# Kernel tuning notes

Hardware: AMD Instinct MI355X
Metric: run time of the kernel (lower is better)

## Reference

```python
import jax, jax.numpy as jnp
import numpy as np

TEMP = 0.3
K_ANCHORS = 512
SK_ITERS = 4  # max_iter=4 in the original; tol early-exit omitted (fixed small iter count)
EPS = 1e-12   # F.normalize clamp_min eps


def setup_inputs() -> dict:
    key = jax.random.key(0)
    k1, k2 = jax.random.split(key)
    x = jax.random.normal(k1, (16, 256, 64, 64), dtype=jnp.float32)
    some_idx = jax.random.randint(k2, (K_ANCHORS,), 0, 64 * 64, dtype=jnp.int32)
    return {"x": x, "some_idx": some_idx}


def sinkhorn_knopp(A):
    # A: [M, k], strictly positive. Normalize by total mass, then alternate
    # L1 column / row normalization (p=1 normalize on positive entries == sum-divide).
    A = A / A.sum()
    def body(A, _):
        A = A / jnp.clip(A.sum(axis=0, keepdims=True), EPS)  # columns
        A = A / jnp.clip(A.sum(axis=1, keepdims=True), EPS)  # rows
        return A, None
    A, _ = jax.lax.scan(body, A, None, length=SK_ITERS)
    return A


def reference(x, some_idx):
    N, C, H, W = x.shape
    k = some_idx.shape[0]
    # L2-normalize over channel dim (F.normalize dim=1)
    l2_x = x / jnp.clip(jnp.linalg.norm(x, axis=1, keepdims=True), EPS)
    # gather k random spatial anchors -> [N, C, k]
    some_x = jnp.take(l2_x.reshape(N, C, H * W), some_idx, axis=-1)
    # cosine scores [N, k, H, W]
    scores = jnp.einsum('nchw,nck->nkhw', l2_x, some_x)
    # flatten to [N*H*W, k], exponentiate, Sinkhorn-Knopp
    A = jnp.exp(scores.transpose(0, 2, 3, 1).reshape(-1, k) / TEMP)
    A = sinkhorn_knopp(A)
    Kmat = A.reshape(N, H, W, k).transpose(0, 3, 1, 2)  # [N, k, H, W]
    # reconstruct from anchors
    return jnp.einsum('nkhw,nck->nchw', Kmat, some_x)
```

## Files before the change

### kernel.cpp

```cpp
#include <hip/hip_runtime.h>
#include <hip/hip_bf16.h>
#include <hip/hip_fp16.h>

#define N_B 16
#define C_DIM 256
#define HW 4096
#define M_TOT (N_B*HW)
#define K_A 512
#define TEMP_INV (1.0f/0.3f)
#define EPS_SK 1e-12f

typedef _Float16 f16x8 __attribute__((ext_vector_type(8)));
typedef _Float16 f16x4 __attribute__((ext_vector_type(4)));
typedef float f32x4 __attribute__((ext_vector_type(4)));

#define GLOBAL_AS __attribute__((address_space(1)))
#define LDS_AS __attribute__((address_space(3)))
__device__ __forceinline__ void gload_lds16(const void* g, void* l){
    __builtin_amdgcn_global_load_lds((GLOBAL_AS const void*)g, (LDS_AS void*)l, 16, 0, 0);
}

__global__ __launch_bounds__(256) void k_normtrans(const float* __restrict__ x,
                                                   _Float16* __restrict__ Lt,
                                                   float* __restrict__ u,
                                                   float* __restrict__ v){
    __shared__ float tl[64][257];
    __shared__ float red[4][64];
    __shared__ float invs[64];
    int n   = blockIdx.x >> 6;
    int hw0 = (blockIdx.x & 63) * 64;
    if (threadIdx.x < 64) u[blockIdx.x*64 + threadIdx.x] = 1.0f;
    if (blockIdx.x < 2)   v[blockIdx.x*256 + threadIdx.x] = 1.0f;
    int tx4 = threadIdx.x & 15;
    int cy  = threadIdx.x >> 4;
    const float* px = x + ((size_t)(n*C_DIM + cy))*HW + hw0 + tx4*4;
    #pragma unroll
    for (int r = 0; r < 16; ++r){
        float4 xv = *(const float4*)(px + (size_t)(r*16)*HW);
        int c = cy + r*16;
        tl[tx4*4+0][c] = xv.x;
        tl[tx4*4+1][c] = xv.y;
        tl[tx4*4+2][c] = xv.z;
        tl[tx4*4+3][c] = xv.w;
    }
    __syncthreads();
    int tx = threadIdx.x & 63, ty = threadIdx.x >> 6;
    float ss = 0.f;
    #pragma unroll
    for (int cc = 0; cc < 64; ++cc){
        float tv = tl[tx][cc*4 + ty];
        ss += tv*tv;
    }
    red[ty][tx] = ss;
    __syncthreads();
    if (ty == 0){
        float s = red[0][tx]+red[1][tx]+red[2][tx]+red[3][tx];
        invs[tx] = 1.0f / fmaxf(sqrtf(s), 1e-12f);
    }
    __syncthreads();
    #pragma unroll
    for (int r = 0; r < 16; ++r){
        int hwl = ty + r*4;
        float inv = invs[hwl];
        float4 a = *(const float4*)&tl[hwl][tx*4];
        f16x4 h;
        h[0] = (_Float16)(a.x*inv); h[1] = (_Float16)(a.y*inv);
        h[2] = (_Float16)(a.z*inv); h[3] = (_Float16)(a.w*inv);
        *(f16x4*)&Lt[((size_t)(n*HW + hw0 + hwl))*C_DIM + tx*4] = h;
    }
}

__global__ __launch_bounds__(256) void k_gather(const _Float16* __restrict__ Lt,
                                                const int* __restrict__ sidx,
                                                _Float16* __restrict__ sxT){
    int n  = blockIdx.y;
    int jj = blockIdx.x*8 + (threadIdx.x >> 5);
    int c8 = (threadIdx.x & 31) * 8;
    int p  = sidx[jj];
    *(f16x8*)&sxT[((size_t)(n*K_A + jj))*C_DIM + c8] =
        *(const f16x8*)&Lt[((size_t)(n*HW + p))*C_DIM + c8];
}

__global__ __launch_bounds__(256) void k_gemm1(const _Float16* __restrict__ Lt,
                                               const _Float16* __restrict__ sxT,
                                               _Float16* __restrict__ A0,
                                               float* __restrict__ part){
    __shared__ _Float16 As[3*128*32];
    __shared__ _Float16 Bs[3*128*32];
    __shared__ float colred[4][128];
    const int swz = (blockIdx.x & 7)*256 + (blockIdx.x >> 3);
    const int jb = swz & 3, mb = (swz >> 2) & 31, nb = swz >> 7;
    const int mbase = mb * 128;
    const int jbase = jb * 128;
    const int t = threadIdx.x;
    const int lane = t & 63, w = t >> 6;
    const int wm = (w >> 1)*64, wn = (w & 1)*64;
    const int l15 = lane & 15, lq = lane >> 4;

    f32x4 acc[4][4] = {};
    const _Float16* pa = Lt  + ((size_t)(nb*HW  + mbase))*C_DIM;
    const _Float16* pb = sxT + ((size_t)(nb*K_A + jbase))*C_DIM;

    const int r0 = t >> 2, ch = t & 3;
    const int r1 = r0 + 64;
    const int cs0 = (ch ^ ((r0 >> 1) & 3)) << 3;
    const int cs1 = (ch ^ ((r1 >> 1) & 3)) << 3;

#define STAGE1(buf, kt) { int k0 = (kt)*32; \
    gload_lds16(pa + (size_t)r0*C_DIM + k0 + cs0, &As[(buf)*4096 + t*8]); \
    gload_lds16(pa + (size_t)r1*C_DIM + k0 + cs1, &As[(buf)*4096 + (256+t)*8]); \
    gload_lds16(pb + (size_t)r0*C_DIM + k0 + cs0, &Bs[(buf)*4096 + t*8]); \
    gload_lds16(pb + (size_t)r1*C_DIM + k0 + cs1, &Bs[(buf)*4096 + (256+t)*8]); }

    STAGE1(0, 0); STAGE1(1, 1); STAGE1(2, 2);
    #pragma unroll
    for (int kt = 0; kt < 8; ++kt){
        if (kt < 6)      asm volatile("s_waitcnt vmcnt(8)" ::: "memory");
        else if (kt < 7) asm volatile("s_waitcnt vmcnt(4)" ::: "memory");
        else             asm volatile("s_waitcnt vmcnt(0)" ::: "memory");
        __builtin_amdgcn_s_barrier();
        __builtin_amdgcn_sched_barrier(0);
        const int cur = kt % 3;
        f16x8 af[4], bf[4];
        #pragma unroll
        for (int mi = 0; mi < 4; ++mi){
            int r = wm + mi*16 + l15;
            af[mi] = *(const f16x8*)&As[cur*4096 + r*32 + ((lq ^ ((r>>1)&3)) << 3)];
        }
        #pragma unroll
        for (int ni = 0; ni < 4; ++ni){
            int r = wn + ni*16 + l15;
            bf[ni] = *(const f16x8*)&Bs[cur*4096 + r*32 + ((lq ^ ((r>>1)&3)) << 3)];
        }
        #pragma unroll
        for (int mi = 0; mi < 4; ++mi)
            #pragma unroll
            for (int ni = 0; ni < 4; ++ni)
                acc[mi][ni] = __builtin_amdgcn_mfma_f32_16x16x32_f16(af[mi], bf[ni], acc[mi][ni], 0, 0, 0);
        __builtin_amdgcn_s_barrier();
        __builtin_amdgcn_sched_barrier(0);
        if (kt < 5) STAGE1((kt+3)%3, kt+3);
    }
    float csum[4] = {0.f, 0.f, 0.f, 0.f};
    #pragma unroll
    for (int mi = 0; mi < 4; ++mi)
        #pragma unroll
        for (int ni = 0; ni < 4; ++ni)
            #pragma unroll
            for (int r = 0; r < 4; ++r){
                int hw = mbase + wm + mi*16 + lq*4 + r;
                int j  = jbase + wn + ni*16 + l15;
                float e = __expf(acc[mi][ni][r] * TEMP_INV);
                A0[((size_t)(nb*HW + hw))*K_A + j] = (_Float16)e;
                csum[ni] += e;
            }
    #pragma unroll
    for (int ni = 0; ni < 4; ++ni){
        float cv = csum[ni];
        cv += __shfl_xor(cv, 16);
        cv += __shfl_xor(cv, 32);
        if (lane < 16) colred[w][wn + ni*16 + l15] = cv;
    }
    __syncthreads();
    if (t < 128){
        int jj = t;
        float s = (jj < 64) ? (colred[0][jj] + colred[2][jj])
                            : (colred[1][jj] + colred[3][jj]);
        part[((size_t)(nb*32 + mb))*K_A + jbase + jj] = s;
    }
}

__global__ __launch_bounds__(64) void k_colfinish(const float* __restrict__ part,
                                                  float* __restrict__ v, int nchunks){
    int j = blockIdx.x;
    int lane = threadIdx.x;
    float s = 0.f;
    for (int r = lane; r < nchunks; r += 64) s += part[(size_t)r*K_A + j];
    #pragma unroll
    for (int off = 32; off; off >>= 1) s += __shfl_xor(s, off);
    if (lane == 0){
        float vo = v[j];
        v[j] = 128.0f * vo / fmaxf(vo * s, EPS_SK);
    }
}

__global__ __launch_bounds__(256) void k_fused(const _Float16* __restrict__ A0,
                                               const float* __restrict__ v,
                                               float* __restrict__ u,
                                               float* __restrict__ part){
    __shared__ float red[4][512];
    int b = blockIdx.x;
    int tg = threadIdx.x >> 6, lane = threadIdx.x & 63;
    float vr[8];
    const float* pv = v + (lane << 3);
    #pragma unroll
    for (int e = 0; e < 8; ++e) vr[e] = pv[e];
    float acc[8] = {};
    for (int it = 0; it < 16; ++it){
        int i = (b << 6) + (it << 2) + tg;
        f16x8 a = *(const f16x8*)&A0[(size_t)i*K_A + (lane << 3)];
        float r = 0.f;
        #pragma unroll
        for (int e = 0; e < 8; ++e) r += (float)a[e] * vr[e];
        #pragma unroll
        for (int off = 32; off; off >>= 1) r += __shfl_xor(r, off);
        float uo = u[i];
        float un = uo / fmaxf(uo * r, EPS_SK);
        if (lane == 0) u[i] = un;
        #pragma unroll
        for (int e = 0; e < 8; ++e) acc[e] += (float)a[e] * un;
    }
    #pragma unroll
    for (int e = 0; e < 8; ++e) red[tg][(lane<<3)+e] = acc[e];
    __syncthreads();
    if (tg == 0){
        #pragma unroll
        for (int e = 0; e < 8; ++e){
            int j = (lane<<3)+e;
            part[((size_t)b)*K_A + j] = red[0][j]+red[1][j]+red[2][j]+red[3][j];
        }
    }
}

__global__ __launch_bounds__(256) void k_sxvT(const _Float16* __restrict__ sxT,
                                              const float* __restrict__ v,
                                              _Float16* __restrict__ SXv){
    __shared__ float tl[64][65];
    int n  = blockIdx.z;
    int j0 = blockIdx.x * 64;
    int c0 = blockIdx.y * 64;
    int tx = threadIdx.x & 63, ty = threadIdx.x >> 6;
    #pragma unroll
    for (int r = 0; r < 16; ++r){
        int jl = ty + r*4;
        tl[jl][tx] = (float)sxT[((size_t)(n*K_A + j0 + jl))*C_DIM + c0 + tx] * v[j0 + jl];
    }
    __syncthreads();
    #pragma unroll
    for (int r = 0; r < 16; ++r){
        int cl = ty + r*4;
        SXv[((size_t)(n*C_DIM + c0 + cl))*K_A + j0 + tx] = (_Float16)tl[tx][cl];
    }
}

__global__ __launch_bounds__(256) void k_gemm2(const _Float16* __restrict__ SXv,
                                               const _Float16* __restrict__ A0,
                                               const float* __restrict__ v,
                                               const float* __restrict__ u,
                                               float* __restrict__ out){
    __shared__ _Float16 As[3*128*32];
    __shared__ _Float16 Bs[3*128*32];
    __shared__ _Float16 vsh[512];
    const int swz = (blockIdx.x & 7)*128 + (blockIdx.x >> 3);
    const int mb = swz & 1, nbi = (swz >> 1) & 31, nb = swz >> 6;
    const int mbase = mb * 128;
    const int nbase = nbi * 128;
    const int t = threadIdx.x;
    const int lane = t & 63, w = t >> 6;
    const int wm = (w >> 1)*64, wn = (w & 1)*64;
    const int l15 = lane & 15, lq = lane >> 4;

    vsh[t]       = (_Float16)v[t];
    vsh[t + 256] = (_Float16)v[t + 256];

    f32x4 acc[4][4] = {};
    f32x4 racc[4] = {};
    const _Float16* pa = SXv + ((size_t)(nb*C_DIM + mbase))*K_A;
    const _Float16* pb = A0  + ((size_t)(nb*HW   + nbase))*K_A;

    const int r0 = t >> 2, ch = t & 3;
    const int r1 = r0 + 64;
    const int cs0 = (ch ^ ((r0 >> 1) & 3)) << 3;
    const int cs1 = (ch ^ ((r1 >> 1) & 3)) << 3;

#define STAGE2(buf, kt) { int k0 = (kt)*32; \
    gload_lds16(pa + (size_t)r0*K_A + k0 + cs0, &As[(buf)*4096 + t*8]); \
    gload_lds16(pa + (size_t)r1*K_A + k0 + cs1, &As[(buf)*4096 + (256+t)*8]); \
    gload_lds16(pb + (size_t)r0*K_A + k0 + cs0, &Bs[(buf)*4096 + t*8]); \
    gload_lds16(pb + (size_t)r1*K_A + k0 + cs1, &Bs[(buf)*4096 + (256+t)*8]); }

    STAGE2(0, 0); STAGE2(1, 1); STAGE2(2, 2);
    #pragma unroll
    for (int kt = 0; kt < 16; ++kt){
        if (kt < 14)      asm volatile("s_waitcnt vmcnt(8)" ::: "memory");
        else if (kt < 15) asm volatile("s_waitcnt vmcnt(4)" ::: "memory");
        else              asm volatile("s_waitcnt vmcnt(0)" ::: "memory");
        __builtin_amdgcn_s_barrier();
        __builtin_amdgcn_sched_barrier(0);
        const int cur = kt % 3;
        f16x8 af[4], bf[4], vf;
        vf = *(const f16x8*)&vsh[kt*32 + lq*8];
        #pragma unroll
        for (int mi = 0; mi < 4; ++mi){
            int r = wm + mi*16 + l15;
            af[mi] = *(const f16x8*)&As[cur*4096 + r*32 + ((lq ^ ((r>>1)&3)) << 3)];
        }
        #pragma unroll
        for (int ni = 0; ni < 4; ++ni){
            int r = wn + ni*16 + l15;
            bf[ni] = *(const f16x8*)&Bs[cur*4096 + r*32 + ((lq ^ ((r>>1)&3)) << 3)];
        }
        #pragma unroll
        for (int mi = 0; mi < 4; ++mi)
            #pragma unroll
            for (int ni = 0; ni < 4; ++ni)
                acc[mi][ni] = __builtin_amdgcn_mfma_f32_16x16x32_f16(af[mi], bf[ni], acc[mi][ni], 0, 0, 0);
        #pragma unroll
        for (int ni = 0; ni < 4; ++ni)
            racc[ni] = __builtin_amdgcn_mfma_f32_16x16x32_f16(vf, bf[ni], racc[ni], 0, 0, 0);
        __builtin_amdgcn_s_barrier();
        __builtin_amdgcn_sched_barrier(0);
        if (kt < 13) STAGE2((kt+3)%3, kt+3);
    }
    float un[4];
    #pragma unroll
    for (int ni = 0; ni < 4; ++ni){
        float rv = racc[ni][0];
        float uo = u[nb*HW + nbase + wn + ni*16 + l15];
        un[ni] = uo / fmaxf(uo * rv, EPS_SK);
    }
    #pragma unroll
    for (int mi = 0; mi < 4; ++mi)
        #pragma unroll
        for (int ni = 0; ni < 4; ++ni)
            #pragma unroll
            for (int r = 0; r < 4; ++r){
                int c  = mbase + wm + mi*16 + lq*4 + r;
                int hw = nbase + wn + ni*16 + l15;
                out[((size_t)(nb*C_DIM + c))*HW + hw] = acc[mi][ni][r] * un[ni];
            }
}

extern "C" void kernel_launch(void* const* d_in, const int* in_sizes, int n_in,
                              void* d_out, int out_size, void* d_ws, size_t ws_size,
                              hipStream_t stream){
    const float* x  = (const float*)d_in[0];
    const int* sidx = (const int*)d_in[1];
    float* out = (float*)d_out;

    char* ws = (char*)d_ws;
    _Float16* Lt  = (_Float16*)ws;  ws += (size_t)N_B*HW*C_DIM*2;
    _Float16* A0  = (_Float16*)ws;  ws += (size_t)M_TOT*K_A*2;
    _Float16* sxT = (_Float16*)ws;  ws += (size_t)N_B*K_A*C_DIM*2;
    _Float16* SXv = (_Float16*)ws;  ws += (size_t)N_B*C_DIM*K_A*2;
    float*    u   = (float*)ws;     ws += (size_t)M_TOT*4;
    float*    v   = (float*)ws;     ws += (size_t)K_A*4;
    float*    part= (float*)ws;     ws += (size_t)1024*K_A*4;

    k_normtrans<<<1024, 256, 0, stream>>>(x, Lt, u, v);
    k_gather   <<<dim3(64,16), 256, 0, stream>>>(Lt, sidx, sxT);
    k_gemm1    <<<2048, 256, 0, stream>>>(Lt, sxT, A0, part);

    k_colfinish<<<512, 64, 0, stream>>>(part, v, 512);
    for (int it = 0; it < 3; ++it){
        k_fused    <<<1024, 256, 0, stream>>>(A0, v, u, part);
        k_colfinish<<<512, 64, 0, stream>>>(part, v, 1024);
    }

    k_sxvT <<<dim3(8,4,16), 256, 0, stream>>>(sxT, v, SXv);
    k_gemm2<<<1024, 256, 0, stream>>>(SXv, A0, v, u, out);
}
```

Measured before the change: 157.4 us.

## Fuse Sinkhorn iterations into one persistent cooperative kernel with grid barriers

Replaces the seven-launch sequence of column-finish and fused row/column passes with a single cooperative kernel. Each of its 512 blocks keeps its 128 rows of A0 in registers across all three iterations and synchronises through a software grid barrier. This removes repeated launch overhead and the re-reading of A0 from memory on every iteration. The cost is heavy register use and the risk that barrier spinning stalls if occupancy falls short, in which case the old launch path is used. It also halves the tile size in the normalize/transpose kernel, doubling its block count and widening its fp16 stores.

```diff
diff --git a/kernel.cpp b/kernel.cpp
--- a/kernel.cpp
+++ b/kernel.cpp
@@ -23,50 +23,55 @@
 __global__ __launch_bounds__(256) void k_normtrans(const float* __restrict__ x,
                                                    _Float16* __restrict__ Lt,
                                                    float* __restrict__ u,
-                                                   float* __restrict__ v){
-    __shared__ float tl[64][257];
-    __shared__ float red[4][64];
-    __shared__ float invs[64];
-    int n   = blockIdx.x >> 6;
-    int hw0 = (blockIdx.x & 63) * 64;
-    if (threadIdx.x < 64) u[blockIdx.x*64 + threadIdx.x] = 1.0f;
+                                                   float* __restrict__ v,
+                                                   unsigned* bcnt, unsigned* bgen){
+    __shared__ float tl[32][257];
+    __shared__ float red[8][32];
+    __shared__ float invs[32];
+    int n   = blockIdx.x >> 7;
+    int hw0 = (blockIdx.x & 127) * 32;
+    if (threadIdx.x < 32) u[blockIdx.x*32 + threadIdx.x] = 1.0f;
     if (blockIdx.x < 2)   v[blockIdx.x*256 + threadIdx.x] = 1.0f;
-    int tx4 = threadIdx.x & 15;
-    int cy  = threadIdx.x >> 4;
+    if (blockIdx.x == 0 && threadIdx.x == 0){
+        __hip_atomic_store(bcnt, 0u, __ATOMIC_RELAXED, __HIP_MEMORY_SCOPE_AGENT);
+        __hip_atomic_store(bgen, 0u, __ATOMIC_RELAXED, __HIP_MEMORY_SCOPE_AGENT);
+    }
+    int tx4 = threadIdx.x & 7;
+    int cy  = threadIdx.x >> 3;
     const float* px = x + ((size_t)(n*C_DIM + cy))*HW + hw0 + tx4*4;
     #pragma unroll
-    for (int r = 0; r < 16; ++r){
-        float4 xv = *(const float4*)(px + (size_t)(r*16)*HW);
-        int c = cy + r*16;
+    for (int r = 0; r < 8; ++r){
+        float4 xv = *(const float4*)(px + (size_t)(r*32)*HW);
+        int c = cy + r*32;
         tl[tx4*4+0][c] = xv.x;
         tl[tx4*4+1][c] = xv.y;
         tl[tx4*4+2][c] = xv.z;
         tl[tx4*4+3][c] = xv.w;
     }
     __syncthreads();
-    int tx = threadIdx.x & 63, ty = threadIdx.x >> 6;
+    int tx = threadIdx.x & 31, ty = threadIdx.x >> 5;
     float ss = 0.f;
     #pragma unroll
-    for (int cc = 0; cc < 64; ++cc){
-        float tv = tl[tx][cc*4 + ty];
+    for (int cc = 0; cc < 32; ++cc){
+        float tv = tl[tx][cc*8 + ty];
         ss += tv*tv;
     }
     red[ty][tx] = ss;
     __syncthreads();
     if (ty == 0){
-        float s = red[0][tx]+red[1][tx]+red[2][tx]+red[3][tx];
+        float s = red[0][tx]+red[1][tx]+red[2][tx]+red[3][tx]
+                + red[4][tx]+red[5][tx]+red[6][tx]+red[7][tx];
         invs[tx] = 1.0f / fmaxf(sqrtf(s), 1e-12f);
     }
     __syncthreads();
     #pragma unroll
-    for (int r = 0; r < 16; ++r){
-        int hwl = ty + r*4;
+    for (int r = 0; r < 4; ++r){
+        int hwl = ty + r*8;
         float inv = invs[hwl];
-        float4 a = *(const float4*)&tl[hwl][tx*4];
-        f16x4 h;
-        h[0] = (_Float16)(a.x*inv); h[1] = (_Float16)(a.y*inv);
-        h[2] = (_Float16)(a.z*inv); h[3] = (_Float16)(a.w*inv);
-        *(f16x4*)&Lt[((size_t)(n*HW + hw0 + hwl))*C_DIM + tx*4] = h;
+        f16x8 h;
+        #pragma unroll
+        for (int e = 0; e < 8; ++e) h[e] = (_Float16)(tl[hwl][tx*8 + e] * inv);
+        *(f16x8*)&Lt[((size_t)(n*HW + hw0 + hwl))*C_DIM + tx*8] = h;
     }
 }
 
@@ -219,6 +224,100 @@
             int j = (lane<<3)+e;
             part[((size_t)b)*K_A + j] = red[0][j]+red[1][j]+red[2][j]+red[3][j];
         }
+    }
+}
+
+__device__ __forceinline__ void gbar(unsigned* cnt, unsigned* gen){
+    __threadfence();
+    __syncthreads();
+    if (threadIdx.x == 0){
+        unsigned g = __hip_atomic_load(gen, __ATOMIC_RELAXED, __HIP_MEMORY_SCOPE_AGENT);
+        unsigned a = __hip_atomic_fetch_add(cnt, 1u, __ATOMIC_ACQ_REL, __HIP_MEMORY_SCOPE_AGENT);
+        if (a == 511u){
+            __hip_atomic_store(cnt, 0u, __ATOMIC_RELAXED, __HIP_MEMORY_SCOPE_AGENT);
+            __hip_atomic_store(gen, g + 1u, __ATOMIC_RELEASE, __HIP_MEMORY_SCOPE_AGENT);
+        } else {
+            while (__hip_atomic_load(gen, __ATOMIC_ACQUIRE, __HIP_MEMORY_SCOPE_AGENT) == g)
+                __builtin_amdgcn_s_sleep(8);
+        }
+    }
+    __syncthreads();
+    __threadfence();
+}
+
+__device__ __forceinline__ void colfin(const float* part, float* v, int b, int t){
+    if (t < 64){
+        float s = 0.f;
+        #pragma unroll
+        for (int g = 0; g < 8; ++g)
+            s += __hip_atomic_load(&part[(size_t)(t + g*64)*K_A + b],
+                                   __ATOMIC_RELAXED, __HIP_MEMORY_SCOPE_AGENT);
+        #pragma unroll
+        for (int off = 32; off; off >>= 1) s += __shfl_xor(s, off);
+        if (t == 0){
+            float vo = __hip_atomic_load(&v[b], __ATOMIC_RELAXED, __HIP_MEMORY_SCOPE_AGENT);
+            __hip_atomic_store(&v[b], 128.0f * vo / fmaxf(vo * s, EPS_SK),
+                               __ATOMIC_RELAXED, __HIP_MEMORY_SCOPE_AGENT);
+        }
+    }
+}
+
+__global__ __launch_bounds__(512, 4) void k_sink(const _Float16* __restrict__ A0,
+                                                 float* v, float* u, float* part,
+                                                 unsigned* bcnt, unsigned* bgen){
+    __shared__ float red[8][512];
+    const int b = blockIdx.x, t = threadIdx.x;
+    const int tg = t >> 6, lane = t & 63;
+    const int i0 = (b << 7) + tg;
+    f16x8 a[16];
+    float ur[16];
+    #pragma unroll
+    for (int it = 0; it < 16; ++it){
+        a[it] = *(const f16x8*)&A0[(size_t)(i0 + it*8)*K_A + (lane<<3)];
+        ur[it] = 1.0f;
+    }
+    colfin(part, v, b, t);
+    gbar(bcnt, bgen);
+    float vr[8];
+    #pragma unroll
+    for (int e = 0; e < 8; ++e)
+        vr[e] = __hip_atomic_load(&v[(lane<<3)+e], __ATOMIC_RELAXED, __HIP_MEMORY_SCOPE_AGENT);
+    for (int t3 = 0; t3 < 3; ++t3){
+        if (t3){
+            gbar(bcnt, bgen);
+            #pragma unroll
+            for (int e = 0; e < 8; ++e)
+                vr[e] = __hip_atomic_load(&v[(lane<<3)+e], __ATOMIC_RELAXED, __HIP_MEMORY_SCOPE_AGENT);
+        }
+        #pragma unroll
+        for (int it = 0; it < 16; ++it){
+            float r = 0.f;
+            #pragma unroll
+            for (int e = 0; e < 8; ++e) r += (float)a[it][e] * vr[e];
+            #pragma unroll
+            for (int off = 32; off; off >>= 1) r += __shfl_xor(r, off);
+            ur[it] = ur[it] / fmaxf(ur[it] * r, EPS_SK);
+        }
+        float acc[8] = {0.f,0.f,0.f,0.f,0.f,0.f,0.f,0.f};
+        #pragma unroll
+        for (int it = 0; it < 16; ++it)
+            #pragma unroll
+            for (int e = 0; e < 8; ++e) acc[e] += (float)a[it][e] * ur[it];
+        #pragma unroll
+        for (int e = 0; e < 8; ++e) red[tg][(lane<<3)+e] = acc[e];
+        __syncthreads();
+        {
+            float s = red[0][t]+red[1][t]+red[2][t]+red[3][t]
+                    + red[4][t]+red[5][t]+red[6][t]+red[7][t];
+            __hip_atomic_store(&part[(size_t)b*K_A + t], s,
+                               __ATOMIC_RELAXED, __HIP_MEMORY_SCOPE_AGENT);
+        }
+        gbar(bcnt, bgen);
+        colfin(part, v, b, t);
+    }
+    if (lane == 0){
+        #pragma unroll
+        for (int it = 0; it < 16; ++it) u[i0 + it*8] = ur[it];
     }
 }
 
@@ -346,15 +445,28 @@
     float*    u   = (float*)ws;     ws += (size_t)M_TOT*4;
     float*    v   = (float*)ws;     ws += (size_t)K_A*4;
     float*    part= (float*)ws;     ws += (size_t)1024*K_A*4;
-
-    k_normtrans<<<1024, 256, 0, stream>>>(x, Lt, u, v);
+    unsigned* bcnt= (unsigned*)ws;  ws += 256;
+    unsigned* bgen= (unsigned*)ws;  ws += 256;
+
+    k_normtrans<<<2048, 256, 0, stream>>>(x, Lt, u, v, bcnt, bgen);
     k_gather   <<<dim3(64,16), 256, 0, stream>>>(Lt, sidx, sxT);
     k_gemm1    <<<2048, 256, 0, stream>>>(Lt, sxT, A0, part);
 
-    k_colfinish<<<512, 64, 0, stream>>>(part, v, 512);
-    for (int it = 0; it < 3; ++it){
-        k_fused    <<<1024, 256, 0, stream>>>(A0, v, u, part);
-        k_colfinish<<<512, 64, 0, stream>>>(part, v, 1024);
+    int occ = 0;
+    hipError_t oe = hipOccupancyMaxActiveBlocksPerMultiprocessor(&occ, k_sink, 512, 0);
+    bool coop = (oe == hipSuccess) && (occ >= 2);
+    if (coop){
+        void* kargs[] = { (void*)&A0, (void*)&v, (void*)&u, (void*)&part,
+                          (void*)&bcnt, (void*)&bgen };
+        coop = (hipLaunchCooperativeKernel((void*)k_sink, dim3(512), dim3(512),
+                                           kargs, 0, stream) == hipSuccess);
+    }
+    if (!coop){
+        k_colfinish<<<512, 64, 0, stream>>>(part, v, 512);
+        for (int it = 0; it < 3; ++it){
+            k_fused    <<<1024, 256, 0, stream>>>(A0, v, u, part);
+            k_colfinish<<<512, 64, 0, stream>>>(part, v, 1024);
+        }
     }
 
     k_sxvT <<<dim3(8,4,16), 256, 0, stream>>>(sxT, v, SXv);
```

Result: no change. 158.1 us (+0.4%).

## Use fp8 copy of exp scores for Sinkhorn iterations and drop row scale vector

Applied to the files above, without the earlier changes.

gemm1 now also writes an fp8 e4m3 copy of the exponentiated score matrix. The Sinkhorn row/column passes read that copy, which halves their memory traffic compared with fp16. The per-row scale u is no longer stored; it is recomputed each iteration as the reciprocal of the row sum, since only the latest row scaling matters. The normalize/transpose kernel uses smaller 32-pixel tiles with 8-wide stores across twice as many blocks. The cost is an extra fp8 write in gemm1 and lower precision in the column sums, which may affect accuracy.

```diff
diff --git a/kernel.cpp b/kernel.cpp
--- a/kernel.cpp
+++ b/kernel.cpp
@@ -1,6 +1,7 @@
 #include <hip/hip_runtime.h>
 #include <hip/hip_bf16.h>
 #include <hip/hip_fp16.h>
+#include <hip/hip_fp8.h>
 
 #define N_B 16
 #define C_DIM 256
@@ -22,51 +23,49 @@
 
 __global__ __launch_bounds__(256) void k_normtrans(const float* __restrict__ x,
                                                    _Float16* __restrict__ Lt,
-                                                   float* __restrict__ u,
                                                    float* __restrict__ v){
-    __shared__ float tl[64][257];
-    __shared__ float red[4][64];
-    __shared__ float invs[64];
-    int n   = blockIdx.x >> 6;
-    int hw0 = (blockIdx.x & 63) * 64;
-    if (threadIdx.x < 64) u[blockIdx.x*64 + threadIdx.x] = 1.0f;
-    if (blockIdx.x < 2)   v[blockIdx.x*256 + threadIdx.x] = 1.0f;
-    int tx4 = threadIdx.x & 15;
-    int cy  = threadIdx.x >> 4;
+    __shared__ float tl[32][257];
+    __shared__ float red[8][32];
+    __shared__ float invs[32];
+    int n   = blockIdx.x >> 7;
+    int hw0 = (blockIdx.x & 127) * 32;
+    if (blockIdx.x < 2) v[blockIdx.x*256 + threadIdx.x] = 1.0f;
+    int tx4 = threadIdx.x & 7;
+    int cy  = threadIdx.x >> 3;
     const float* px = x + ((size_t)(n*C_DIM + cy))*HW + hw0 + tx4*4;
     #pragma unroll
-    for (int r = 0; r < 16; ++r){
-        float4 xv = *(const float4*)(px + (size_t)(r*16)*HW);
-        int c = cy + r*16;
+    for (int r = 0; r < 8; ++r){
+        float4 xv = *(const float4*)(px + (size_t)(r*32)*HW);
+        int c = cy + r*32;
         tl[tx4*4+0][c] = xv.x;
         tl[tx4*4+1][c] = xv.y;
         tl[tx4*4+2][c] = xv.z;
         tl[tx4*4+3][c] = xv.w;
     }
     __syncthreads();
-    int tx = threadIdx.x & 63, ty = threadIdx.x >> 6;
+    int tx = threadIdx.x & 31, ty = threadIdx.x >> 5;
     float ss = 0.f;
     #pragma unroll
-    for (int cc = 0; cc < 64; ++cc){
-        float tv = tl[tx][cc*4 + ty];
+    for (int cc = 0; cc < 32; ++cc){
+        float tv = tl[tx][cc*8 + ty];
         ss += tv*tv;
     }
     red[ty][tx] = ss;
     __syncthreads();
     if (ty == 0){
-        float s = red[0][tx]+red[1][tx]+red[2][tx]+red[3][tx];
+        float s = red[0][tx]+red[1][tx]+red[2][tx]+red[3][tx]
+                + red[4][tx]+red[5][tx]+red[6][tx]+red[7][tx];
         invs[tx] = 1.0f / fmaxf(sqrtf(s), 1e-12f);
     }
     __syncthreads();
     #pragma unroll
-    for (int r = 0; r < 16; ++r){
-        int hwl = ty + r*4;
+    for (int r = 0; r < 4; ++r){
+        int hwl = ty + r*8;
         float inv = invs[hwl];
-        float4 a = *(const float4*)&tl[hwl][tx*4];
-        f16x4 h;
-        h[0] = (_Float16)(a.x*inv); h[1] = (_Float16)(a.y*inv);
-        h[2] = (_Float16)(a.z*inv); h[3] = (_Float16)(a.w*inv);
-        *(f16x4*)&Lt[((size_t)(n*HW + hw0 + hwl))*C_DIM + tx*4] = h;
+        f16x8 h;
+        #pragma unroll
+        for (int e = 0; e < 8; ++e) h[e] = (_Float16)(tl[hwl][tx*8 + e] * inv);
+        *(f16x8*)&Lt[((size_t)(n*HW + hw0 + hwl))*C_DIM + tx*8] = h;
     }
 }
 
@@ -84,6 +83,7 @@
 __global__ __launch_bounds__(256) void k_gemm1(const _Float16* __restrict__ Lt,
                                                const _Float16* __restrict__ sxT,
                                                _Float16* __restrict__ A0,
+                                               __hip_fp8_e4m3* __restrict__ A8,
                                                float* __restrict__ part){
     __shared__ _Float16 As[3*128*32];
     __shared__ _Float16 Bs[3*128*32];
@@ -151,7 +151,9 @@
                 int hw = mbase + wm + mi*16 + lq*4 + r;
                 int j  = jbase + wn + ni*16 + l15;
                 float e = __expf(acc[mi][ni][r] * TEMP_INV);
-                A0[((size_t)(nb*HW + hw))*K_A + j] = (_Float16)e;
+                size_t idx = ((size_t)(nb*HW + hw))*K_A + j;
+                A0[idx] = (_Float16)e;
+                A8[idx] = __hip_fp8_e4m3(e);
                 csum[ni] += e;
             }
     #pragma unroll
@@ -184,10 +186,9 @@
     }
 }
 
-__global__ __launch_bounds__(256) void k_fused(const _Float16* __restrict__ A0,
-                                               const float* __restrict__ v,
-                                               float* __restrict__ u,
-                                               float* __restrict__ part){
+__global__ __launch_bounds__(256) void k_fused8(const __hip_fp8_e4m3* __restrict__ A8,
+                                                const float* __restrict__ v,
+                                                float* __restrict__ part){
     __shared__ float red[4][512];
     int b = blockIdx.x;
     int tg = threadIdx.x >> 6, lane = threadIdx.x & 63;
@@ -196,19 +197,22 @@
     #pragma unroll
     for (int e = 0; e < 8; ++e) vr[e] = pv[e];
     float acc[8] = {};
+    union U8 { uint2 u; __hip_fp8_e4m3 f8[8]; };
     for (int it = 0; it < 16; ++it){
         int i = (b << 6) + (it << 2) + tg;
-        f16x8 a = *(const f16x8*)&A0[(size_t)i*K_A + (lane << 3)];
+        U8 a;
+        a.u = *(const uint2*)&A8[(size_t)i*K_A + (lane << 3)];
+        float av[8];
+        #pragma unroll
+        for (int e = 0; e < 8; ++e) av[e] = (float)a.f8[e];
         float r = 0.f;
         #pragma unroll
-        for (int e = 0; e < 8; ++e) r += (float)a[e] * vr[e];
+        for (int e = 0; e < 8; ++e) r += av[e] * vr[e];
         #pragma unroll
         for (int off = 32; off; off >>= 1) r += __shfl_xor(r, off);
-        float uo = u[i];
-        float un = uo / fmaxf(uo * r, EPS_SK);
-        if (lane == 0) u[i] = un;
-        #pragma unroll
-        for (int e = 0; e < 8; ++e) acc[e] += (float)a[e] * un;
+        float un = 1.0f / fmaxf(r, EPS_SK);
+        #pragma unroll
+        for (int e = 0; e < 8; ++e) acc[e] += av[e] * un;
     }
     #pragma unroll
     for (int e = 0; e < 8; ++e) red[tg][(lane<<3)+e] = acc[e];
@@ -246,7 +250,6 @@
 __global__ __launch_bounds__(256) void k_gemm2(const _Float16* __restrict__ SXv,
                                                const _Float16* __restrict__ A0,
                                                const float* __restrict__ v,
-                                               const float* __restrict__ u,
                                                float* __restrict__ out){
     __shared__ _Float16 As[3*128*32];
     __shared__ _Float16 Bs[3*128*32];
@@ -314,11 +317,8 @@
     }
     float un[4];
     #pragma unroll
-    for (int ni = 0; ni < 4; ++ni){
-        float rv = racc[ni][0];
-        float uo = u[nb*HW + nbase + wn + ni*16 + l15];
-        un[ni] = uo / fmaxf(uo * rv, EPS_SK);
-    }
+    for (int ni = 0; ni < 4; ++ni)
+        un[ni] = 1.0f / fmaxf(racc[ni][0], EPS_SK);
     #pragma unroll
     for (int mi = 0; mi < 4; ++mi)
         #pragma unroll
@@ -339,24 +339,24 @@
     float* out = (float*)d_out;
 
     char* ws = (char*)d_ws;
-    _Float16* Lt  = (_Float16*)ws;  ws += (size_t)N_B*HW*C_DIM*2;
-    _Float16* A0  = (_Float16*)ws;  ws += (size_t)M_TOT*K_A*2;
-    _Float16* sxT = (_Float16*)ws;  ws += (size_t)N_B*K_A*C_DIM*2;
-    _Float16* SXv = (_Float16*)ws;  ws += (size_t)N_B*C_DIM*K_A*2;
-    float*    u   = (float*)ws;     ws += (size_t)M_TOT*4;
-    float*    v   = (float*)ws;     ws += (size_t)K_A*4;
-    float*    part= (float*)ws;     ws += (size_t)1024*K_A*4;
-
-    k_normtrans<<<1024, 256, 0, stream>>>(x, Lt, u, v);
+    _Float16* Lt  = (_Float16*)ws;        ws += (size_t)N_B*HW*C_DIM*2;
+    _Float16* A0  = (_Float16*)ws;        ws += (size_t)M_TOT*K_A*2;
+    __hip_fp8_e4m3* A8 = (__hip_fp8_e4m3*)ws; ws += (size_t)M_TOT*K_A;
+    _Float16* sxT = (_Float16*)ws;        ws += (size_t)N_B*K_A*C_DIM*2;
+    _Float16* SXv = (_Float16*)ws;        ws += (size_t)N_B*C_DIM*K_A*2;
+    float*    v   = (float*)ws;           ws += (size_t)K_A*4;
+    float*    part= (float*)ws;           ws += (size_t)1024*K_A*4;
+
+    k_normtrans<<<2048, 256, 0, stream>>>(x, Lt, v);
     k_gather   <<<dim3(64,16), 256, 0, stream>>>(Lt, sidx, sxT);
-    k_gemm1    <<<2048, 256, 0, stream>>>(Lt, sxT, A0, part);
+    k_gemm1    <<<2048, 256, 0, stream>>>(Lt, sxT, A0, A8, part);
 
     k_colfinish<<<512, 64, 0, stream>>>(part, v, 512);
     for (int it = 0; it < 3; ++it){
-        k_fused    <<<1024, 256, 0, stream>>>(A0, v, u, part);
+        k_fused8   <<<1024, 256, 0, stream>>>(A8, v, part);
         k_colfinish<<<512, 64, 0, stream>>>(part, v, 1024);
     }
 
     k_sxvT <<<dim3(8,4,16), 256, 0, stream>>>(sxT, v, SXv);
-    k_gemm2<<<1024, 256, 0, stream>>>(SXv, A0, v, u, out);
-}
+    k_gemm2<<<1024, 256, 0, stream>>>(SXv, A0, v, out);
+}
```

Measured after the change: 162.7 us. 1.03x slower.
